# Performance work log

Hardware: AMD Instinct MI355X
Metric: run time of the kernel (lower is better)

Reference implementation:

```python
import jax, jax.numpy as jnp
import numpy as np

DIM = 512
HEADS = 8
WINDOW = 128


def setup_inputs() -> dict:
    key = jax.random.key(0)
    k1, k2, k3, k4 = jax.random.split(key, 4)
    x = jax.random.normal(k1, (16, 4096, DIM), dtype=jnp.float32)
    w_qkv = jax.random.normal(k2, (3 * DIM, DIM), dtype=jnp.float32) * 0.02
    w_proj = jax.random.normal(k3, (DIM, DIM), dtype=jnp.float32) * 0.02
    b_proj = jax.random.normal(k4, (DIM,), dtype=jnp.float32) * 0.02
    return {"x": x, "w_qkv": w_qkv, "w_proj": w_proj, "b_proj": b_proj}


def reference(x, w_qkv, w_proj, b_proj):
    B0, T0, C = x.shape
    H = HEADS
    hd = C // H
    scale = hd ** (-0.5)
    W = WINDOW
    # split into independent windows: [B*T/W, W, C]
    xw = x.reshape(-1, W, C)
    Bw = xw.shape[0]
    # qkv projection (no bias), reshape to [3, Bw, H, W, hd]
    qkv = (xw @ w_qkv.T).reshape(Bw, W, 3, H, hd).transpose(2, 0, 3, 1, 4)
    q, k, v = qkv[0], qkv[1], qkv[2]
    # scaled scores per window: [Bw, H, W, W]
    attn = jnp.einsum("bhqd,bhkd->bhqk", q, k) * scale
    causal_mask = jnp.tril(jnp.ones((W, W), dtype=bool))
    attn = jnp.where(causal_mask, attn, -jnp.inf)
    attn = jax.nn.softmax(attn, axis=-1)
    out = jnp.einsum("bhqk,bhkd->bhqd", attn, v)  # [Bw, H, W, hd]
    out = out.transpose(0, 2, 1, 3).reshape(Bw, W, C)
    out = out @ w_proj.T + b_proj
    return out.reshape(B0, T0, C)
```

## Files before the change

kernel.cpp:

```cpp
#include <hip/hip_runtime.h>
#include <stdint.h>


typedef unsigned short ushort_t;
typedef __attribute__((ext_vector_type(8))) short short8;
typedef __attribute__((ext_vector_type(4))) float f32x4;
typedef __attribute__((ext_vector_type(4))) float f4v;
typedef __attribute__((ext_vector_type(4))) unsigned short us4;

static __device__ __forceinline__ unsigned short f2bf(float f) {
  unsigned int u = __float_as_uint(f);
  u += 0x7FFFu + ((u >> 16) & 1u);
  return (unsigned short)(u >> 16);
}

static __device__ __forceinline__ void gl_lds16(const ushort_t* g, ushort_t* l) {
  __builtin_amdgcn_global_load_lds(
      (const __attribute__((address_space(1))) void*)g,
      (__attribute__((address_space(3))) void*)l, 16, 0, 0);
}

__global__ __launch_bounds__(256) void cast_f32_bf16(const float* __restrict__ in,
                                                     ushort_t* __restrict__ out, int n4) {
  int i = blockIdx.x * 256 + threadIdx.x;
  if (i >= n4) return;
  f4v v = ((const f4v*)in)[i];
  us4 o;
  o.x = f2bf(v.x); o.y = f2bf(v.y); o.z = f2bf(v.z); o.w = f2bf(v.w);
  ((us4*)out)[i] = o;
}

__global__ __launch_bounds__(512, 2) void qkv_gemm(const ushort_t* __restrict__ A,
                                                   const ushort_t* __restrict__ B,
                                                   ushort_t* __restrict__ qk,
                                                   ushort_t* __restrict__ vT) {
  __shared__ __align__(16) ushort_t smem[3 * 24576];
  const int tid = threadIdx.x;
  const int lane = tid & 63;
  const int wv = tid >> 6;
  const int wr = wv >> 1, wc = wv & 1;
  const int lr = lane & 15;
  const int lg = lane >> 4;

  const int bid = blockIdx.x;
  const int wg = (bid & 7) * 384 + (bid >> 3);
  const int nb = wg % 12;
  const int mb = wg / 12;
  const int m0 = mb << 8;
  const int n0 = nb << 7;

  const int srow = tid >> 3;
  const int ssw  = (((tid & 7) ^ (srow & 7)) << 3);
  const ushort_t* gA = A + (size_t)(m0 + srow) * 512 + ssw;
  const ushort_t* gB = B + (size_t)(n0 + srow) * 512 + ssw;

  f32x4 acc[4][4] = {};

  auto STAGE = [&](int t, int q) {
    ushort_t* Ab = smem + q * 24576;
    ushort_t* Bb = Ab + 16384;
    const int kk = t << 6;
#pragma unroll
    for (int r = 0; r < 4; ++r)
      gl_lds16(gA + (size_t)(r * 64) * 512 + kk, Ab + (r * 512 + wv * 64) * 8);
#pragma unroll
    for (int r = 0; r < 2; ++r)
      gl_lds16(gB + (size_t)(r * 64) * 512 + kk, Bb + (r * 512 + wv * 64) * 8);
  };

  STAGE(0, 0);
  STAGE(1, 1);
  asm volatile("s_waitcnt vmcnt(6)" ::: "memory");
  __builtin_amdgcn_s_barrier();

#pragma unroll
  for (int t = 0; t < 8; ++t) {
    const ushort_t* Ab = smem + (t % 3) * 24576;
    const ushort_t* Bb = Ab + 16384;
    short8 a[4][2], b[4][2];
#pragma unroll
    for (int ks = 0; ks < 2; ++ks) {
      const int co = ((((ks << 2) | lg) ^ (lr & 7)) << 3);
#pragma unroll
      for (int mi = 0; mi < 4; ++mi)
        a[mi][ks] = *(const short8*)(Ab + (wr * 64 + mi * 16 + lr) * 64 + co);
#pragma unroll
      for (int ni = 0; ni < 4; ++ni)
        b[ni][ks] = *(const short8*)(Bb + (wc * 64 + ni * 16 + lr) * 64 + co);
    }
    if (t + 2 < 8) STAGE(t + 2, (t + 2) % 3);
    if (t < 7) {
      if (t + 2 < 8) asm volatile("s_waitcnt vmcnt(6)" ::: "memory");
      else           asm volatile("s_waitcnt vmcnt(0)" ::: "memory");
      asm volatile("s_waitcnt lgkmcnt(0)" ::: "memory");
      __builtin_amdgcn_s_barrier();
    }
    __builtin_amdgcn_s_setprio(1);
#pragma unroll
    for (int ks = 0; ks < 2; ++ks)
#pragma unroll
      for (int mi = 0; mi < 4; ++mi)
#pragma unroll
        for (int ni = 0; ni < 4; ++ni)
          acc[mi][ni] = __builtin_amdgcn_mfma_f32_16x16x32_bf16(a[mi][ks], b[ni][ks], acc[mi][ni], 0, 0, 0);
    __builtin_amdgcn_s_setprio(0);
  }

  const int lg4 = lg << 2;
  if (n0 < 1024) {
#pragma unroll
    for (int mi = 0; mi < 4; ++mi) {
      const int rbase = m0 + wr * 64 + mi * 16 + lg4;
#pragma unroll
      for (int ni = 0; ni < 4; ++ni) {
        const int col = n0 + wc * 64 + ni * 16 + lr;
#pragma unroll
        for (int rg = 0; rg < 4; ++rg)
          qk[(size_t)(rbase + rg) * 1024 + col] = f2bf(acc[mi][ni][rg]);
      }
    }
  } else {
    const int winb = (m0 >> 7) + (wr >> 1);
    const int t0b = (wr & 1) * 64;
#pragma unroll
    for (int mi = 0; mi < 4; ++mi) {
      const int t0 = t0b + mi * 16 + lg4;
#pragma unroll
      for (int ni = 0; ni < 4; ++ni) {
        const int c = n0 - 1024 + wc * 64 + ni * 16 + lr;
        const int h = c >> 6, d = c & 63;
        us4 o;
        o.x = f2bf(acc[mi][ni][0]); o.y = f2bf(acc[mi][ni][1]);
        o.z = f2bf(acc[mi][ni][2]); o.w = f2bf(acc[mi][ni][3]);
        *(us4*)(vT + (size_t)((winb * 8 + h) * 64 + d) * 128 + t0) = o;
      }
    }
  }
}

__global__ __launch_bounds__(256) void attn_kernel(const ushort_t* __restrict__ qk,
                                                   const ushort_t* __restrict__ vT,
                                                   ushort_t* __restrict__ attn_out) {
  __shared__ __align__(16) ushort_t smem[24576];
  ushort_t* qs = smem;
  ushort_t* ks_ = smem + 8192;
  ushort_t* vs = smem + 16384;
  ushort_t* ps = smem;

  const int tid = threadIdx.x;
  const int lane = tid & 63;
  const int wv = tid >> 6;
  const int win = blockIdx.x >> 3;
  const int h = blockIdx.x & 7;
  const int lr = lane & 15;
  const int lg = lane >> 4;
  const int lg4 = lg << 2;
  const int sw = lr & 7;

  const size_t qbase = (size_t)win * 128 * 1024 + h * 64;
#pragma unroll
  for (int r = 0; r < 4; ++r) {
    const int g = r * 256 + tid;
    const int t = g >> 3, ch = g & 7;
    short8 vq = *(const short8*)(qk + qbase + (size_t)t * 1024 + ch * 8);
    short8 vk = *(const short8*)(qk + qbase + 512 + (size_t)t * 1024 + ch * 8);
    const int st = t * 64 + ((ch ^ (t & 7)) << 3);
    *(short8*)(qs + st) = vq;
    *(short8*)(ks_ + st) = vk;
  }
  const size_t vbase = (size_t)(win * 8 + h) * 64 * 128;
#pragma unroll
  for (int r = 0; r < 4; ++r) {
    const int g = r * 256 + tid;
    const int d = g >> 4, ch = g & 15;
    short8 vvv = *(const short8*)(vT + vbase + (size_t)d * 128 + ch * 8);
    *(short8*)(vs + d * 128 + ((ch ^ (d & 7)) << 3)) = vvv;
  }
  __syncthreads();

  const int rt[2] = {wv, 7 - wv};

  f32x4 sacc[2][8] = {};
#pragma unroll
  for (int ks2 = 0; ks2 < 2; ++ks2) {
    const int co = ((((ks2 << 2) | lg) ^ sw) << 3);
    short8 a0 = *(const short8*)(qs + (rt[0] * 16 + lr) * 64 + co);
    short8 a1 = *(const short8*)(qs + (rt[1] * 16 + lr) * 64 + co);
#pragma unroll
    for (int ni = 0; ni < 8; ++ni) {
      if (ni <= rt[1]) {
        short8 b = *(const short8*)(ks_ + (ni * 16 + lr) * 64 + co);
        if (ni <= rt[0])
          sacc[0][ni] = __builtin_amdgcn_mfma_f32_16x16x32_bf16(a0, b, sacc[0][ni], 0, 0, 0);
        sacc[1][ni] = __builtin_amdgcn_mfma_f32_16x16x32_bf16(a1, b, sacc[1][ni], 0, 0, 0);
      }
    }
  }

  __syncthreads();

  const float C = 0.125f * 1.44269504f;
#pragma unroll
  for (int mi = 0; mi < 2; ++mi) {
    const int r = rt[mi];
    const int rb = r * 16;
#pragma unroll
    for (int ni = 0; ni < 8; ++ni) {
      if (ni <= r) {
#pragma unroll
        for (int rg = 0; rg < 4; ++rg) {
          const int row = rb + lg4 + rg;
          const int col = ni * 16 + lr;
          float e = __builtin_exp2f(sacc[mi][ni][rg] * C);
          e = (col <= row) ? e : 0.0f;
          ps[row * 128 + ((((col >> 3) ^ (row & 7)) << 3) | (col & 7))] = f2bf(e);
        }
      }
    }
    if (!(r & 1)) {
      const int col = (r + 1) * 16 + lr;
#pragma unroll
      for (int rg = 0; rg < 4; ++rg) {
        const int row = rb + lg4 + rg;
        ps[row * 128 + ((((col >> 3) ^ (row & 7)) << 3) | (col & 7))] = 0;
      }
    }
  }

  const short one_bf = (short)0x3F80;
  short8 ones;
#pragma unroll
  for (int j = 0; j < 8; ++j) ones[j] = (lr == 0) ? one_bf : (short)0;

  f32x4 oacc[2][4] = {};
  f32x4 sm[2] = {};
#pragma unroll
  for (int ks2 = 0; ks2 < 4; ++ks2) {
    const int co = ((((ks2 << 2) | lg) ^ sw) << 3);
    if (ks2 <= (rt[1] >> 1)) {
      short8 b[4];
#pragma unroll
      for (int nd = 0; nd < 4; ++nd)
        b[nd] = *(const short8*)(vs + (nd * 16 + lr) * 128 + co);
      short8 a1 = *(const short8*)(ps + (rt[1] * 16 + lr) * 128 + co);
#pragma unroll
      for (int nd = 0; nd < 4; ++nd)
        oacc[1][nd] = __builtin_amdgcn_mfma_f32_16x16x32_bf16(a1, b[nd], oacc[1][nd], 0, 0, 0);
      sm[1] = __builtin_amdgcn_mfma_f32_16x16x32_bf16(a1, ones, sm[1], 0, 0, 0);
      if (ks2 <= (rt[0] >> 1)) {
        short8 a0 = *(const short8*)(ps + (rt[0] * 16 + lr) * 128 + co);
#pragma unroll
        for (int nd = 0; nd < 4; ++nd)
          oacc[0][nd] = __builtin_amdgcn_mfma_f32_16x16x32_bf16(a0, b[nd], oacc[0][nd], 0, 0, 0);
        sm[0] = __builtin_amdgcn_mfma_f32_16x16x32_bf16(a0, ones, sm[0], 0, 0, 0);
      }
    }
  }

  const int src = lane & 48;
  const size_t obase = (size_t)win * 128 * 512 + h * 64;
#pragma unroll
  for (int mi = 0; mi < 2; ++mi) {
    const int rb = rt[mi] * 16;
    float rsv[4];
#pragma unroll
    for (int rg = 0; rg < 4; ++rg)
      rsv[rg] = 1.0f / __shfl(sm[mi][rg], src);
#pragma unroll
    for (int nd = 0; nd < 4; ++nd)
#pragma unroll
      for (int rg = 0; rg < 4; ++rg) {
        const int row = rb + lg4 + rg;
        const int col = nd * 16 + lr;
        attn_out[obase + (size_t)row * 512 + col] = f2bf(oacc[mi][nd][rg] * rsv[rg]);
      }
  }
}

__global__ __launch_bounds__(512, 2) void proj_gemm(const ushort_t* __restrict__ A,
                                                    const ushort_t* __restrict__ B,
                                                    const float* __restrict__ bias,
                                                    float* __restrict__ out) {
  __shared__ __align__(16) ushort_t smem[3 * 24576];
  const int tid = threadIdx.x;
  const int lane = tid & 63;
  const int wv = tid >> 6;
  const int wr = wv >> 1, wc = wv & 1;
  const int lr = lane & 15;
  const int lg = lane >> 4;

  const int bid = blockIdx.x;
  const int wg = (bid & 7) * 128 + (bid >> 3);
  const int nb = wg & 3;
  const int mb = wg >> 2;
  const int m0 = mb << 8;
  const int n0 = nb << 7;

  const int srow = tid >> 3;
  const int ssw  = (((tid & 7) ^ (srow & 7)) << 3);
  const ushort_t* gA = A + (size_t)(m0 + srow) * 512 + ssw;
  const ushort_t* gB = B + (size_t)(n0 + srow) * 512 + ssw;

  f32x4 acc[4][4] = {};

  auto STAGE = [&](int t, int q) {
    ushort_t* Ab = smem + q * 24576;
    ushort_t* Bb = Ab + 16384;
    const int kk = t << 6;
#pragma unroll
    for (int r = 0; r < 4; ++r)
      gl_lds16(gA + (size_t)(r * 64) * 512 + kk, Ab + (r * 512 + wv * 64) * 8);
#pragma unroll
    for (int r = 0; r < 2; ++r)
      gl_lds16(gB + (size_t)(r * 64) * 512 + kk, Bb + (r * 512 + wv * 64) * 8);
  };

  STAGE(0, 0);
  STAGE(1, 1);
  asm volatile("s_waitcnt vmcnt(6)" ::: "memory");
  __builtin_amdgcn_s_barrier();

#pragma unroll
  for (int t = 0; t < 8; ++t) {
    const ushort_t* Ab = smem + (t % 3) * 24576;
    const ushort_t* Bb = Ab + 16384;
    short8 a[4][2], b[4][2];
#pragma unroll
    for (int ks = 0; ks < 2; ++ks) {
      const int co = ((((ks << 2) | lg) ^ (lr & 7)) << 3);
#pragma unroll
      for (int mi = 0; mi < 4; ++mi)
        a[mi][ks] = *(const short8*)(Ab + (wr * 64 + mi * 16 + lr) * 64 + co);
#pragma unroll
      for (int ni = 0; ni < 4; ++ni)
        b[ni][ks] = *(const short8*)(Bb + (wc * 64 + ni * 16 + lr) * 64 + co);
    }
    if (t + 2 < 8) STAGE(t + 2, (t + 2) % 3);
    if (t < 7) {
      if (t + 2 < 8) asm volatile("s_waitcnt vmcnt(6)" ::: "memory");
      else           asm volatile("s_waitcnt vmcnt(0)" ::: "memory");
      asm volatile("s_waitcnt lgkmcnt(0)" ::: "memory");
      __builtin_amdgcn_s_barrier();
    }
    __builtin_amdgcn_s_setprio(1);
#pragma unroll
    for (int ks = 0; ks < 2; ++ks)
#pragma unroll
      for (int mi = 0; mi < 4; ++mi)
#pragma unroll
        for (int ni = 0; ni < 4; ++ni)
          acc[mi][ni] = __builtin_amdgcn_mfma_f32_16x16x32_bf16(a[mi][ks], b[ni][ks], acc[mi][ni], 0, 0, 0);
    __builtin_amdgcn_s_setprio(0);
  }

  const int lg4 = lg << 2;
#pragma unroll
  for (int mi = 0; mi < 4; ++mi) {
    const int rbase = m0 + wr * 64 + mi * 16 + lg4;
#pragma unroll
    for (int ni = 0; ni < 4; ++ni) {
      const int col = n0 + wc * 64 + ni * 16 + lr;
      const float bv = bias[col];
#pragma unroll
      for (int rg = 0; rg < 4; ++rg)
        out[(size_t)(rbase + rg) * 512 + col] = acc[mi][ni][rg] + bv;
    }
  }
}

extern "C" void kernel_launch(void* const* d_in, const int* in_sizes, int n_in,
                              void* d_out, int out_size, void* d_ws, size_t ws_size,
                              hipStream_t stream) {
  const float* x      = (const float*)d_in[0];
  const float* w_qkv  = (const float*)d_in[1];
  const float* w_proj = (const float*)d_in[2];
  const float* b_proj = (const float*)d_in[3];
  float* out = (float*)d_out;

  char* ws = (char*)d_ws;
  ushort_t* x_bf     = (ushort_t*)(ws);
  ushort_t* qk_ws    = (ushort_t*)(ws + 67108864);
  ushort_t* vT_ws    = (ushort_t*)(ws + 67108864 + 134217728);
  ushort_t* attn_ws  = (ushort_t*)(ws + 67108864 + 134217728 + 67108864);
  ushort_t* wqkv_bf  = (ushort_t*)(ws + 335544320);
  ushort_t* wproj_bf = (ushort_t*)(ws + 337117184);

  cast_f32_bf16<<<32768, 256, 0, stream>>>(x, x_bf, 8388608);
  cast_f32_bf16<<<768, 256, 0, stream>>>(w_qkv, wqkv_bf, 196608);
  cast_f32_bf16<<<256, 256, 0, stream>>>(w_proj, wproj_bf, 65536);

  qkv_gemm<<<3072, 512, 0, stream>>>(x_bf, wqkv_bf, qk_ws, vT_ws);
  attn_kernel<<<4096, 256, 0, stream>>>(qk_ws, vT_ws, attn_ws);
  proj_gemm<<<1024, 512, 0, stream>>>(attn_ws, wproj_bf, b_proj, out);
}
```

Measured before the change: 477.0 us.

## Fuse windowed attention with output projection, one block per window

Replaces the separate attention and projection kernels with one kernel. Each 512-thread block handles one 128-token window and loops over the 8 heads. For each head it computes causal attention into LDS, then accumulates that head's slice of the output projection into registers. This removes the write and re-read of the intermediate bf16 attention tensor and one launch. In exchange the grid drops to 512 large blocks with 128KB of LDS each, giving low occupancy and no overlap between global loads and compute across heads. Load balance also varies, since each wave owns a causal row band.

New measurement: 956.6 us. 101% more time.

```diff
diff --git a/kernel.cpp b/kernel.cpp
--- a/kernel.cpp
+++ b/kernel.cpp
@@ -138,228 +138,165 @@
   }
 }
 
-__global__ __launch_bounds__(256) void attn_kernel(const ushort_t* __restrict__ qk,
-                                                   const ushort_t* __restrict__ vT,
-                                                   ushort_t* __restrict__ attn_out) {
-  __shared__ __align__(16) ushort_t smem[24576];
-  ushort_t* qs = smem;
-  ushort_t* ks_ = smem + 8192;
-  ushort_t* vs = smem + 16384;
-  ushort_t* ps = smem;
+__global__ __launch_bounds__(512) void fused_attn_proj(const ushort_t* __restrict__ qk,
+                                                       const ushort_t* __restrict__ vT,
+                                                       const ushort_t* __restrict__ wproj,
+                                                       const float* __restrict__ bias,
+                                                       float* __restrict__ out) {
+  __shared__ __align__(16) ushort_t smem[65536];
+  ushort_t* Ks = smem;
+  ushort_t* Vs = smem + 8192;
+  ushort_t* Bs = smem + 16384;
+  ushort_t* Ps = smem + 49152;
 
   const int tid = threadIdx.x;
   const int lane = tid & 63;
   const int wv = tid >> 6;
-  const int win = blockIdx.x >> 3;
-  const int h = blockIdx.x & 7;
+  const int wr2 = wv >> 2;
+  const int wc2 = wv & 3;
   const int lr = lane & 15;
   const int lg = lane >> 4;
   const int lg4 = lg << 2;
   const int sw = lr & 7;
 
-  const size_t qbase = (size_t)win * 128 * 1024 + h * 64;
-#pragma unroll
-  for (int r = 0; r < 4; ++r) {
-    const int g = r * 256 + tid;
-    const int t = g >> 3, ch = g & 7;
-    short8 vq = *(const short8*)(qk + qbase + (size_t)t * 1024 + ch * 8);
-    short8 vk = *(const short8*)(qk + qbase + 512 + (size_t)t * 1024 + ch * 8);
-    const int st = t * 64 + ((ch ^ (t & 7)) << 3);
-    *(short8*)(qs + st) = vq;
-    *(short8*)(ks_ + st) = vk;
+  const int win = (blockIdx.x & 7) * 64 + (blockIdx.x >> 3);
+  const int w128 = win * 128;
+  const size_t qrow = (size_t)w128 * 1024;
+  const size_t vbase = (size_t)win * 8 * 8192;
+
+  f32x4 acc[4][8] = {};
+
+  for (int h = 0; h < 8; ++h) {
+    __syncthreads();
+
+#pragma unroll
+    for (int i = 0; i < 2; ++i) {
+      const int g = wv * 128 + i * 64 + lane;
+      const int t = g >> 3, ch = g & 7;
+      gl_lds16(qk + qrow + (size_t)t * 1024 + 512 + h * 64 + ((ch ^ (t & 7)) << 3),
+               Ks + (wv * 128 + i * 64) * 8);
+    }
+#pragma unroll
+    for (int i = 0; i < 2; ++i) {
+      const int g = wv * 128 + i * 64 + lane;
+      const int d = g >> 4, ch = g & 15;
+      gl_lds16(vT + vbase + (size_t)h * 8192 + d * 128 + ((ch ^ (d & 7)) << 3),
+               Vs + (wv * 128 + i * 64) * 8);
+    }
+#pragma unroll
+    for (int i = 0; i < 8; ++i) {
+      const int g = wv * 512 + i * 64 + lane;
+      const int j = g >> 3, ch = g & 7;
+      gl_lds16(wproj + (size_t)j * 512 + h * 64 + ((ch ^ (j & 7)) << 3),
+               Bs + (wv * 512 + i * 64) * 8);
+    }
+    short8 aq[2];
+#pragma unroll
+    for (int ks = 0; ks < 2; ++ks)
+      aq[ks] = *(const short8*)(qk + qrow + (size_t)(wv * 16 + lr) * 1024 + h * 64 + ks * 32 + lg * 8);
+
+    __syncthreads();
+
+    f32x4 sacc[8] = {};
+#pragma unroll
+    for (int ks = 0; ks < 2; ++ks) {
+      const int co = ((((ks << 2) | lg) ^ sw) << 3);
+#pragma unroll
+      for (int ni = 0; ni < 8; ++ni) {
+        if (ni <= wv) {
+          short8 kb = *(const short8*)(Ks + (ni * 16 + lr) * 64 + co);
+          sacc[ni] = __builtin_amdgcn_mfma_f32_16x16x32_bf16(aq[ks], kb, sacc[ni], 0, 0, 0);
+        }
+      }
+    }
+
+    const float C = 0.125f * 1.44269504f;
+#pragma unroll
+    for (int ni = 0; ni < 8; ++ni) {
+      if (ni <= wv) {
+#pragma unroll
+        for (int rg = 0; rg < 4; ++rg) {
+          const int row = wv * 16 + lg4 + rg;
+          const int col = ni * 16 + lr;
+          float e = __builtin_exp2f(sacc[ni][rg] * C);
+          e = (col <= row) ? e : 0.0f;
+          Ps[row * 128 + ((((col >> 3) ^ (row & 7)) << 3) | (col & 7))] = f2bf(e);
+        }
+      }
+    }
+    if (!(wv & 1)) {
+      const int col = (wv + 1) * 16 + lr;
+#pragma unroll
+      for (int rg = 0; rg < 4; ++rg) {
+        const int row = wv * 16 + lg4 + rg;
+        Ps[row * 128 + ((((col >> 3) ^ (row & 7)) << 3) | (col & 7))] = 0;
+      }
+    }
+
+    const short one_bf = (short)0x3F80;
+    short8 ones;
+#pragma unroll
+    for (int j = 0; j < 8; ++j) ones[j] = (lr == 0) ? one_bf : (short)0;
+
+    f32x4 oacc[4] = {};
+    f32x4 sm = {};
+#pragma unroll
+    for (int ks2 = 0; ks2 < 4; ++ks2) {
+      if (ks2 <= (wv >> 1)) {
+        const int co = ((((ks2 << 2) | lg) ^ sw) << 3);
+        short8 pa = *(const short8*)(Ps + (wv * 16 + lr) * 128 + co);
+#pragma unroll
+        for (int nd = 0; nd < 4; ++nd) {
+          short8 vb = *(const short8*)(Vs + (nd * 16 + lr) * 128 + co);
+          oacc[nd] = __builtin_amdgcn_mfma_f32_16x16x32_bf16(pa, vb, oacc[nd], 0, 0, 0);
+        }
+        sm = __builtin_amdgcn_mfma_f32_16x16x32_bf16(pa, ones, sm, 0, 0, 0);
+      }
+    }
+
+    const int src = lane & 48;
+    float rsv[4];
+#pragma unroll
+    for (int rg = 0; rg < 4; ++rg)
+      rsv[rg] = 1.0f / __shfl(sm[rg], src);
+#pragma unroll
+    for (int nd = 0; nd < 4; ++nd)
+#pragma unroll
+      for (int rg = 0; rg < 4; ++rg) {
+        const int row = wv * 16 + lg4 + rg;
+        const int col = nd * 16 + lr;
+        Ps[row * 128 + ((((col >> 3) ^ (row & 7)) << 3) | (col & 7))] =
+            f2bf(oacc[nd][rg] * rsv[rg]);
+      }
+
+    __syncthreads();
+
+#pragma unroll
+    for (int ks = 0; ks < 2; ++ks) {
+      const int co = ((((ks << 2) | lg) ^ sw) << 3);
+      short8 pa[4], pb[8];
+#pragma unroll
+      for (int mi = 0; mi < 4; ++mi)
+        pa[mi] = *(const short8*)(Ps + (wr2 * 64 + mi * 16 + lr) * 128 + co);
+#pragma unroll
+      for (int ni = 0; ni < 8; ++ni)
+        pb[ni] = *(const short8*)(Bs + (wc2 * 128 + ni * 16 + lr) * 64 + co);
+      __builtin_amdgcn_s_setprio(1);
+#pragma unroll
+      for (int mi = 0; mi < 4; ++mi)
+#pragma unroll
+        for (int ni = 0; ni < 8; ++ni)
+          acc[mi][ni] = __builtin_amdgcn_mfma_f32_16x16x32_bf16(pa[mi], pb[ni], acc[mi][ni], 0, 0, 0);
+      __builtin_amdgcn_s_setprio(0);
+    }
   }
-  const size_t vbase = (size_t)(win * 8 + h) * 64 * 128;
-#pragma unroll
-  for (int r = 0; r < 4; ++r) {
-    const int g = r * 256 + tid;
-    const int d = g >> 4, ch = g & 15;
-    short8 vvv = *(const short8*)(vT + vbase + (size_t)d * 128 + ch * 8);
-    *(short8*)(vs + d * 128 + ((ch ^ (d & 7)) << 3)) = vvv;
-  }
-  __syncthreads();
-
-  const int rt[2] = {wv, 7 - wv};
-
-  f32x4 sacc[2][8] = {};
-#pragma unroll
-  for (int ks2 = 0; ks2 < 2; ++ks2) {
-    const int co = ((((ks2 << 2) | lg) ^ sw) << 3);
-    short8 a0 = *(const short8*)(qs + (rt[0] * 16 + lr) * 64 + co);
-    short8 a1 = *(const short8*)(qs + (rt[1] * 16 + lr) * 64 + co);
+
+#pragma unroll
+  for (int mi = 0; mi < 4; ++mi) {
+    const int rbase = w128 + wr2 * 64 + mi * 16 + lg4;
 #pragma unroll
     for (int ni = 0; ni < 8; ++ni) {
-      if (ni <= rt[1]) {
-        short8 b = *(const short8*)(ks_ + (ni * 16 + lr) * 64 + co);
-        if (ni <= rt[0])
-          sacc[0][ni] = __builtin_amdgcn_mfma_f32_16x16x32_bf16(a0, b, sacc[0][ni], 0, 0, 0);
-        sacc[1][ni] = __builtin_amdgcn_mfma_f32_16x16x32_bf16(a1, b, sacc[1][ni], 0, 0, 0);
-      }
-    }
-  }
-
-  __syncthreads();
-
-  const float C = 0.125f * 1.44269504f;
-#pragma unroll
-  for (int mi = 0; mi < 2; ++mi) {
-    const int r = rt[mi];
-    const int rb = r * 16;
-#pragma unroll
-    for (int ni = 0; ni < 8; ++ni) {
-      if (ni <= r) {
-#pragma unroll
-        for (int rg = 0; rg < 4; ++rg) {
-          const int row = rb + lg4 + rg;
-          const int col = ni * 16 + lr;
-          float e = __builtin_exp2f(sacc[mi][ni][rg] * C);
-          e = (col <= row) ? e : 0.0f;
-          ps[row * 128 + ((((col >> 3) ^ (row & 7)) << 3) | (col & 7))] = f2bf(e);
-        }
-      }
-    }
-    if (!(r & 1)) {
-      const int col = (r + 1) * 16 + lr;
-#pragma unroll
-      for (int rg = 0; rg < 4; ++rg) {
-        const int row = rb + lg4 + rg;
-        ps[row * 128 + ((((col >> 3) ^ (row & 7)) << 3) | (col & 7))] = 0;
-      }
-    }
-  }
-
-  const short one_bf = (short)0x3F80;
-  short8 ones;
-#pragma unroll
-  for (int j = 0; j < 8; ++j) ones[j] = (lr == 0) ? one_bf : (short)0;
-
-  f32x4 oacc[2][4] = {};
-  f32x4 sm[2] = {};
-#pragma unroll
-  for (int ks2 = 0; ks2 < 4; ++ks2) {
-    const int co = ((((ks2 << 2) | lg) ^ sw) << 3);
-    if (ks2 <= (rt[1] >> 1)) {
-      short8 b[4];
-#pragma unroll
-      for (int nd = 0; nd < 4; ++nd)
-        b[nd] = *(const short8*)(vs + (nd * 16 + lr) * 128 + co);
-      short8 a1 = *(const short8*)(ps + (rt[1] * 16 + lr) * 128 + co);
-#pragma unroll
-      for (int nd = 0; nd < 4; ++nd)
-        oacc[1][nd] = __builtin_amdgcn_mfma_f32_16x16x32_bf16(a1, b[nd], oacc[1][nd], 0, 0, 0);
-      sm[1] = __builtin_amdgcn_mfma_f32_16x16x32_bf16(a1, ones, sm[1], 0, 0, 0);
-      if (ks2 <= (rt[0] >> 1)) {
-        short8 a0 = *(const short8*)(ps + (rt[0] * 16 + lr) * 128 + co);
-#pragma unroll
-        for (int nd = 0; nd < 4; ++nd)
-          oacc[0][nd] = __builtin_amdgcn_mfma_f32_16x16x32_bf16(a0, b[nd], oacc[0][nd], 0, 0, 0);
-        sm[0] = __builtin_amdgcn_mfma_f32_16x16x32_bf16(a0, ones, sm[0], 0, 0, 0);
-      }
-    }
-  }
-
-  const int src = lane & 48;
-  const size_t obase = (size_t)win * 128 * 512 + h * 64;
-#pragma unroll
-  for (int mi = 0; mi < 2; ++mi) {
-    const int rb = rt[mi] * 16;
-    float rsv[4];
-#pragma unroll
-    for (int rg = 0; rg < 4; ++rg)
-      rsv[rg] = 1.0f / __shfl(sm[mi][rg], src);
-#pragma unroll
-    for (int nd = 0; nd < 4; ++nd)
-#pragma unroll
-      for (int rg = 0; rg < 4; ++rg) {
-        const int row = rb + lg4 + rg;
-        const int col = nd * 16 + lr;
-        attn_out[obase + (size_t)row * 512 + col] = f2bf(oacc[mi][nd][rg] * rsv[rg]);
-      }
-  }
-}
-
-__global__ __launch_bounds__(512, 2) void proj_gemm(const ushort_t* __restrict__ A,
-                                                    const ushort_t* __restrict__ B,
-                                                    const float* __restrict__ bias,
-                                                    float* __restrict__ out) {
-  __shared__ __align__(16) ushort_t smem[3 * 24576];
-  const int tid = threadIdx.x;
-  const int lane = tid & 63;
-  const int wv = tid >> 6;
-  const int wr = wv >> 1, wc = wv & 1;
-  const int lr = lane & 15;
-  const int lg = lane >> 4;
-
-  const int bid = blockIdx.x;
-  const int wg = (bid & 7) * 128 + (bid >> 3);
-  const int nb = wg & 3;
-  const int mb = wg >> 2;
-  const int m0 = mb << 8;
-  const int n0 = nb << 7;
-
-  const int srow = tid >> 3;
-  const int ssw  = (((tid & 7) ^ (srow & 7)) << 3);
-  const ushort_t* gA = A + (size_t)(m0 + srow) * 512 + ssw;
-  const ushort_t* gB = B + (size_t)(n0 + srow) * 512 + ssw;
-
-  f32x4 acc[4][4] = {};
-
-  auto STAGE = [&](int t, int q) {
-    ushort_t* Ab = smem + q * 24576;
-    ushort_t* Bb = Ab + 16384;
-    const int kk = t << 6;
-#pragma unroll
-    for (int r = 0; r < 4; ++r)
-      gl_lds16(gA + (size_t)(r * 64) * 512 + kk, Ab + (r * 512 + wv * 64) * 8);
-#pragma unroll
-    for (int r = 0; r < 2; ++r)
-      gl_lds16(gB + (size_t)(r * 64) * 512 + kk, Bb + (r * 512 + wv * 64) * 8);
-  };
-
-  STAGE(0, 0);
-  STAGE(1, 1);
-  asm volatile("s_waitcnt vmcnt(6)" ::: "memory");
-  __builtin_amdgcn_s_barrier();
-
-#pragma unroll
-  for (int t = 0; t < 8; ++t) {
-    const ushort_t* Ab = smem + (t % 3) * 24576;
-    const ushort_t* Bb = Ab + 16384;
-    short8 a[4][2], b[4][2];
-#pragma unroll
-    for (int ks = 0; ks < 2; ++ks) {
-      const int co = ((((ks << 2) | lg) ^ (lr & 7)) << 3);
-#pragma unroll
-      for (int mi = 0; mi < 4; ++mi)
-        a[mi][ks] = *(const short8*)(Ab + (wr * 64 + mi * 16 + lr) * 64 + co);
-#pragma unroll
-      for (int ni = 0; ni < 4; ++ni)
-        b[ni][ks] = *(const short8*)(Bb + (wc * 64 + ni * 16 + lr) * 64 + co);
-    }
-    if (t + 2 < 8) STAGE(t + 2, (t + 2) % 3);
-    if (t < 7) {
-      if (t + 2 < 8) asm volatile("s_waitcnt vmcnt(6)" ::: "memory");
-      else           asm volatile("s_waitcnt vmcnt(0)" ::: "memory");
-      asm volatile("s_waitcnt lgkmcnt(0)" ::: "memory");
-      __builtin_amdgcn_s_barrier();
-    }
-    __builtin_amdgcn_s_setprio(1);
-#pragma unroll
-    for (int ks = 0; ks < 2; ++ks)
-#pragma unroll
-      for (int mi = 0; mi < 4; ++mi)
-#pragma unroll
-        for (int ni = 0; ni < 4; ++ni)
-          acc[mi][ni] = __builtin_amdgcn_mfma_f32_16x16x32_bf16(a[mi][ks], b[ni][ks], acc[mi][ni], 0, 0, 0);
-    __builtin_amdgcn_s_setprio(0);
-  }
-
-  const int lg4 = lg << 2;
-#pragma unroll
-  for (int mi = 0; mi < 4; ++mi) {
-    const int rbase = m0 + wr * 64 + mi * 16 + lg4;
-#pragma unroll
-    for (int ni = 0; ni < 4; ++ni) {
-      const int col = n0 + wc * 64 + ni * 16 + lr;
+      const int col = wc2 * 128 + ni * 16 + lr;
       const float bv = bias[col];
 #pragma unroll
       for (int rg = 0; rg < 4; ++rg)
@@ -381,7 +318,6 @@
   ushort_t* x_bf     = (ushort_t*)(ws);
   ushort_t* qk_ws    = (ushort_t*)(ws + 67108864);
   ushort_t* vT_ws    = (ushort_t*)(ws + 67108864 + 134217728);
-  ushort_t* attn_ws  = (ushort_t*)(ws + 67108864 + 134217728 + 67108864);
   ushort_t* wqkv_bf  = (ushort_t*)(ws + 335544320);
   ushort_t* wproj_bf = (ushort_t*)(ws + 337117184);
 
@@ -390,6 +326,5 @@
   cast_f32_bf16<<<256, 256, 0, stream>>>(w_proj, wproj_bf, 65536);
 
   qkv_gemm<<<3072, 512, 0, stream>>>(x_bf, wqkv_bf, qk_ws, vT_ws);
-  attn_kernel<<<4096, 256, 0, stream>>>(qk_ws, vT_ws, attn_ws);
-  proj_gemm<<<1024, 512, 0, stream>>>(attn_ws, wproj_bf, b_proj, out);
-}
+  fused_attn_proj<<<512, 512, 0, stream>>>(qk_ws, vT_ws, wproj_bf, b_proj, out);
+}
```

## Store Q/K head-major per window and load K/V via direct global-to-LDS

Applied to the files above, without the earlier changes.

The QKV GEMM epilogue now writes Q and K into separate head-contiguous buffers laid out [window, head, t, d] instead of a row-interleaved qk matrix. This makes each attention block's Q/K tile contiguous. The attention kernel loads K and V with global_load_lds, reading the source pre-swizzled, and loads Q fragments straight into registers instead of staging them in LDS. The P tile is remapped into the freed LDS region. In exchange, the GEMM epilogue's scalar stores become more scattered across windows and heads, and all Q fragments are read directly from global memory.

Result: no change. 480.4 us (+0.7%).

```diff
diff --git a/kernel.cpp b/kernel.cpp
--- a/kernel.cpp
+++ b/kernel.cpp
@@ -32,7 +32,8 @@
 
 __global__ __launch_bounds__(512, 2) void qkv_gemm(const ushort_t* __restrict__ A,
                                                    const ushort_t* __restrict__ B,
-                                                   ushort_t* __restrict__ qk,
+                                                   ushort_t* __restrict__ q_ws,
+                                                   ushort_t* __restrict__ k_ws,
                                                    ushort_t* __restrict__ vT) {
   __shared__ __align__(16) ushort_t smem[3 * 24576];
   const int tid = threadIdx.x;
@@ -108,15 +109,21 @@
 
   const int lg4 = lg << 2;
   if (n0 < 1024) {
+    ushort_t* dst = (n0 < 512) ? q_ws : k_ws;
+    const int cbase = (n0 < 512) ? n0 : (n0 - 512);
 #pragma unroll
     for (int mi = 0; mi < 4; ++mi) {
-      const int rbase = m0 + wr * 64 + mi * 16 + lg4;
+      const int rr0 = wr * 64 + mi * 16 + lg4;
 #pragma unroll
       for (int ni = 0; ni < 4; ++ni) {
-        const int col = n0 + wc * 64 + ni * 16 + lr;
-#pragma unroll
-        for (int rg = 0; rg < 4; ++rg)
-          qk[(size_t)(rbase + rg) * 1024 + col] = f2bf(acc[mi][ni][rg]);
+        const int c = cbase + wc * 64 + ni * 16 + lr;
+        const int h = c >> 6, d = c & 63;
+#pragma unroll
+        for (int rg = 0; rg < 4; ++rg) {
+          const int rr = rr0 + rg;
+          const int win = (m0 >> 7) + (rr >> 7);
+          dst[(size_t)(win * 8 + h) * 8192 + (rr & 127) * 64 + d] = f2bf(acc[mi][ni][rg]);
+        }
       }
     }
   } else {
@@ -138,14 +145,13 @@
   }
 }
 
-__global__ __launch_bounds__(256) void attn_kernel(const ushort_t* __restrict__ qk,
+__global__ __launch_bounds__(256) void attn_kernel(const ushort_t* __restrict__ q_ws,
+                                                   const ushort_t* __restrict__ k_ws,
                                                    const ushort_t* __restrict__ vT,
                                                    ushort_t* __restrict__ attn_out) {
   __shared__ __align__(16) ushort_t smem[24576];
-  ushort_t* qs = smem;
-  ushort_t* ks_ = smem + 8192;
-  ushort_t* vs = smem + 16384;
-  ushort_t* ps = smem;
+  ushort_t* ks_ = smem;
+  ushort_t* vs = smem + 8192;
 
   const int tid = threadIdx.x;
   const int lane = tid & 63;
@@ -157,42 +163,39 @@
   const int lg4 = lg << 2;
   const int sw = lr & 7;
 
-  const size_t qbase = (size_t)win * 128 * 1024 + h * 64;
-#pragma unroll
-  for (int r = 0; r < 4; ++r) {
-    const int g = r * 256 + tid;
+  const size_t base = (size_t)(win * 8 + h) * 8192;
+
+#pragma unroll
+  for (int i = 0; i < 4; ++i) {
+    const int g = i * 256 + tid;
     const int t = g >> 3, ch = g & 7;
-    short8 vq = *(const short8*)(qk + qbase + (size_t)t * 1024 + ch * 8);
-    short8 vk = *(const short8*)(qk + qbase + 512 + (size_t)t * 1024 + ch * 8);
-    const int st = t * 64 + ((ch ^ (t & 7)) << 3);
-    *(short8*)(qs + st) = vq;
-    *(short8*)(ks_ + st) = vk;
-  }
-  const size_t vbase = (size_t)(win * 8 + h) * 64 * 128;
-#pragma unroll
-  for (int r = 0; r < 4; ++r) {
-    const int g = r * 256 + tid;
-    const int d = g >> 4, ch = g & 15;
-    short8 vvv = *(const short8*)(vT + vbase + (size_t)d * 128 + ch * 8);
-    *(short8*)(vs + d * 128 + ((ch ^ (d & 7)) << 3)) = vvv;
-  }
+    gl_lds16(k_ws + base + t * 64 + ((ch ^ (t & 7)) << 3), ks_ + g * 8);
+    const int d = g >> 4, ch2 = g & 15;
+    gl_lds16(vT + base + d * 128 + ((ch2 ^ (d & 7)) << 3), vs + g * 8);
+  }
+
+  const int rt[2] = {wv, 7 - wv};
+
+  short8 aq[2][2];
+#pragma unroll
+  for (int mi = 0; mi < 2; ++mi)
+#pragma unroll
+    for (int ks = 0; ks < 2; ++ks)
+      aq[mi][ks] = *(const short8*)(q_ws + base + (size_t)(rt[mi] * 16 + lr) * 64 + ks * 32 + lg * 8);
+
   __syncthreads();
-
-  const int rt[2] = {wv, 7 - wv};
 
   f32x4 sacc[2][8] = {};
 #pragma unroll
   for (int ks2 = 0; ks2 < 2; ++ks2) {
     const int co = ((((ks2 << 2) | lg) ^ sw) << 3);
-    short8 a0 = *(const short8*)(qs + (rt[0] * 16 + lr) * 64 + co);
-    short8 a1 = *(const short8*)(qs + (rt[1] * 16 + lr) * 64 + co);
 #pragma unroll
     for (int ni = 0; ni < 8; ++ni) {
       if (ni <= rt[1]) {
         short8 b = *(const short8*)(ks_ + (ni * 16 + lr) * 64 + co);
         if (ni <= rt[0])
-          sacc[0][ni] = __builtin_amdgcn_mfma_f32_16x16x32_bf16(a0, b, sacc[0][ni], 0, 0, 0);
-        sacc[1][ni] = __builtin_amdgcn_mfma_f32_16x16x32_bf16(a1, b, sacc[1][ni], 0, 0, 0);
+          sacc[0][ni] = __builtin_amdgcn_mfma_f32_16x16x32_bf16(aq[0][ks2], b, sacc[0][ni], 0, 0, 0);
+        sacc[1][ni] = __builtin_amdgcn_mfma_f32_16x16x32_bf16(aq[1][ks2], b, sacc[1][ni], 0, 0, 0);
       }
     }
   }
@@ -213,7 +216,8 @@
           const int col = ni * 16 + lr;
           float e = __builtin_exp2f(sacc[mi][ni][rg] * C);
           e = (col <= row) ? e : 0.0f;
-          ps[row * 128 + ((((col >> 3) ^ (row & 7)) << 3) | (col & 7))] = f2bf(e);
+          smem[(row & 63) * 128 + ((row >> 6) << 14) +
+               ((((col >> 3) ^ (row & 7)) << 3) | (col & 7))] = f2bf(e);
         }
       }
     }
@@ -222,7 +226,8 @@
 #pragma unroll
       for (int rg = 0; rg < 4; ++rg) {
         const int row = rb + lg4 + rg;
-        ps[row * 128 + ((((col >> 3) ^ (row & 7)) << 3) | (col & 7))] = 0;
+        smem[(row & 63) * 128 + ((row >> 6) << 14) +
+             ((((col >> 3) ^ (row & 7)) << 3) | (col & 7))] = 0;
       }
     }
   }
@@ -231,6 +236,11 @@
   short8 ones;
 #pragma unroll
   for (int j = 0; j < 8; ++j) ones[j] = (lr == 0) ? one_bf : (short)0;
+
+  const int r0 = rt[0] * 16 + lr;
+  const int r1 = rt[1] * 16 + lr;
+  const ushort_t* p0 = smem + (r0 & 63) * 128 + ((r0 >> 6) << 14);
+  const ushort_t* p1 = smem + (r1 & 63) * 128 + ((r1 >> 6) << 14);
 
   f32x4 oacc[2][4] = {};
   f32x4 sm[2] = {};
@@ -242,13 +252,13 @@
 #pragma unroll
       for (int nd = 0; nd < 4; ++nd)
         b[nd] = *(const short8*)(vs + (nd * 16 + lr) * 128 + co);
-      short8 a1 = *(const short8*)(ps + (rt[1] * 16 + lr) * 128 + co);
+      short8 a1 = *(const short8*)(p1 + co);
 #pragma unroll
       for (int nd = 0; nd < 4; ++nd)
         oacc[1][nd] = __builtin_amdgcn_mfma_f32_16x16x32_bf16(a1, b[nd], oacc[1][nd], 0, 0, 0);
       sm[1] = __builtin_amdgcn_mfma_f32_16x16x32_bf16(a1, ones, sm[1], 0, 0, 0);
       if (ks2 <= (rt[0] >> 1)) {
-        short8 a0 = *(const short8*)(ps + (rt[0] * 16 + lr) * 128 + co);
+        short8 a0 = *(const short8*)(p0 + co);
 #pragma unroll
         for (int nd = 0; nd < 4; ++nd)
           oacc[0][nd] = __builtin_amdgcn_mfma_f32_16x16x32_bf16(a0, b[nd], oacc[0][nd], 0, 0, 0);
@@ -379,9 +389,10 @@
 
   char* ws = (char*)d_ws;
   ushort_t* x_bf     = (ushort_t*)(ws);
-  ushort_t* qk_ws    = (ushort_t*)(ws + 67108864);
-  ushort_t* vT_ws    = (ushort_t*)(ws + 67108864 + 134217728);
-  ushort_t* attn_ws  = (ushort_t*)(ws + 67108864 + 134217728 + 67108864);
+  ushort_t* q_ws     = (ushort_t*)(ws + 67108864);
+  ushort_t* k_ws     = (ushort_t*)(ws + 134217728);
+  ushort_t* vT_ws    = (ushort_t*)(ws + 201326592);
+  ushort_t* attn_ws  = (ushort_t*)(ws + 268435456);
   ushort_t* wqkv_bf  = (ushort_t*)(ws + 335544320);
   ushort_t* wproj_bf = (ushort_t*)(ws + 337117184);
 
@@ -389,7 +400,7 @@
   cast_f32_bf16<<<768, 256, 0, stream>>>(w_qkv, wqkv_bf, 196608);
   cast_f32_bf16<<<256, 256, 0, stream>>>(w_proj, wproj_bf, 65536);
 
-  qkv_gemm<<<3072, 512, 0, stream>>>(x_bf, wqkv_bf, qk_ws, vT_ws);
-  attn_kernel<<<4096, 256, 0, stream>>>(qk_ws, vT_ws, attn_ws);
+  qkv_gemm<<<3072, 512, 0, stream>>>(x_bf, wqkv_bf, q_ws, k_ws, vT_ws);
+  attn_kernel<<<4096, 256, 0, stream>>>(q_ws, k_ws, vT_ws, attn_ws);
   proj_gemm<<<1024, 512, 0, stream>>>(attn_ws, wproj_bf, b_proj, out);
 }
```
